# Kernel tuning notes

Measured on AMD Instinct MI355X. Metric: run time of the kernel, lower is better.

Reference implementation:

```python
import jax, jax.numpy as jnp
import numpy as np

N_NODES = 100000
N_EDGES = 1_600_000
F_IN, HID, N_CLS = 128, 64, 32
NEG_SLOPE = 0.2  # PyG GATv2Conv default


def _segment_softmax(scores, seg, num_segments):
    # numerically stable softmax over edges grouped by destination node
    m = jax.ops.segment_max(scores, seg, num_segments=num_segments)
    ex = jnp.exp(scores - m[seg])
    s = jax.ops.segment_sum(ex, seg, num_segments=num_segments)
    return ex / (s[seg] + 1e-16)


def _gatv2_layer(x, src, dst, Wl, bl, Wr, br, att, bias, num_nodes):
    xl = x @ Wl + bl              # source transform  [N, C]
    xr = x @ Wr + br              # target transform  [N, C]
    # per-edge GATv2 attention logit: a . leaky_relu(xl_j + xr_i)
    e = jax.nn.leaky_relu(xl[src] + xr[dst], NEG_SLOPE) @ att  # [E]
    alpha = _segment_softmax(e, dst, num_nodes)                 # [E]
    out = jax.ops.segment_sum(alpha[:, None] * xl[src], dst, num_segments=num_nodes)
    return out + bias


def _add_self_loops(edge_index, n):
    loops = jnp.arange(n, dtype=edge_index.dtype)
    return jnp.concatenate([edge_index, jnp.stack([loops, loops])], axis=1)


def setup_inputs() -> dict:
    key = jax.random.key(0)
    ks = jax.random.split(key, 8)
    s1 = 1.0 / np.sqrt(F_IN)
    s2 = 1.0 / np.sqrt(HID)
    return {
        "x": jax.random.normal(ks[0], (N_NODES, F_IN), jnp.float32),
        "edge_index": jax.random.randint(ks[1], (2, N_EDGES), 0, N_NODES, jnp.int64),
        "W1l": jax.random.normal(ks[2], (F_IN, HID), jnp.float32) * s1,
        "b1l": jnp.zeros((HID,), jnp.float32),
        "W1r": jax.random.normal(ks[3], (F_IN, HID), jnp.float32) * s1,
        "b1r": jnp.zeros((HID,), jnp.float32),
        "att1": jax.random.normal(ks[4], (HID,), jnp.float32) * s2,
        "bias1": jnp.zeros((HID,), jnp.float32),
        "W2l": jax.random.normal(ks[5], (HID, N_CLS), jnp.float32) * s2,
        "b2l": jnp.zeros((N_CLS,), jnp.float32),
        "W2r": jax.random.normal(ks[6], (HID, N_CLS), jnp.float32) * s2,
        "b2r": jnp.zeros((N_CLS,), jnp.float32),
        "att2": jax.random.normal(ks[7], (N_CLS,), jnp.float32) / np.sqrt(N_CLS),
        "bias2": jnp.zeros((N_CLS,), jnp.float32),
    }


def reference(x, edge_index, W1l, b1l, W1r, b1r, att1, bias1,
              W2l, b2l, W2r, b2r, att2, bias2):
    n = x.shape[0]
    ei = _add_self_loops(edge_index, n)
    src, dst = ei[0], ei[1]
    h = jax.nn.relu(_gatv2_layer(x, src, dst, W1l, b1l, W1r, b1r, att1, bias1, n))
    # F.dropout(training=False) is identity in eval mode
    out = _gatv2_layer(h, src, dst, W2l, b2l, W2r, b2r, att2, bias2, n)
    return out
```

## Files before the change

kernel.cpp:

```cpp
#include <hip/hip_runtime.h>
#include <math.h>

#define F_IN 128
#define HID 64
#define NCLS 32
#define NEG 0.2f
#define NBKT 256
#define CHUNK 8192

__device__ __forceinline__ void f4fma(float4& a, float s, const float4& w) {
    a.x = fmaf(s, w.x, a.x);
    a.y = fmaf(s, w.y, a.y);
    a.z = fmaf(s, w.z, a.z);
    a.w = fmaf(s, w.w, a.w);
}
__device__ __forceinline__ unsigned short f2bf(float f) {
    unsigned u = __float_as_uint(f);
    return (unsigned short)((u + 0x7FFFu + ((u >> 16) & 1u)) >> 16);
}
__device__ __forceinline__ float bf2f(unsigned short s) {
    return __uint_as_float(((unsigned)s) << 16);
}


__global__ __launch_bounds__(256) void zeroBuckets(int* __restrict__ bucketSize, int BK) {
    int i = blockIdx.x * 256 + threadIdx.x;
    if (i < BK) bucketSize[i] = 0;
}

__global__ __launch_bounds__(256) void bucketHist(const int* __restrict__ ei,
                                                  int Eorig, int Etot,
                                                  int* __restrict__ bucketSize, int BK) {
    __shared__ int h[512];
    int t = threadIdx.x;
    for (int j = t; j < BK; j += 256) h[j] = 0;
    __syncthreads();
    int base = blockIdx.x * CHUNK;
    int end = base + CHUNK < Etot ? base + CHUNK : Etot;
    for (int i = base + t; i < end; i += 256) {
        int dst = i < Eorig ? ei[Eorig + i] : i - Eorig;
        atomicAdd(&h[dst >> 8], 1);
    }
    __syncthreads();
    for (int j = t; j < BK; j += 256)
        if (h[j]) atomicAdd(&bucketSize[j], h[j]);
}

__global__ __launch_bounds__(256) void bucketScan(const int* __restrict__ bucketSize,
                                                  int* __restrict__ bucketStart,
                                                  int* __restrict__ bucketCursor,
                                                  int BK, int Etot) {
    __shared__ int sd[256];
    int t = threadIdx.x;
    int v0 = (2 * t     < BK) ? bucketSize[2 * t]     : 0;
    int v1 = (2 * t + 1 < BK) ? bucketSize[2 * t + 1] : 0;
    int ts = v0 + v1;
    sd[t] = ts;
    __syncthreads();
    for (int off = 1; off < 256; off <<= 1) {
        int x = (t >= off) ? sd[t - off] : 0;
        __syncthreads();
        sd[t] += x;
        __syncthreads();
    }
    int excl = sd[t] - ts;
    if (2 * t < BK)     { bucketStart[2 * t] = excl;          bucketCursor[2 * t] = excl; }
    if (2 * t + 1 < BK) { bucketStart[2 * t + 1] = excl + v0; bucketCursor[2 * t + 1] = excl + v0; }
    if (t == 255) bucketStart[BK] = Etot;
}

__global__ __launch_bounds__(256) void bucketScatter(const int* __restrict__ ei,
                                                     int Eorig, int Etot,
                                                     int* __restrict__ bucketCursor,
                                                     int2* __restrict__ pairs, int BK) {
    __shared__ int h[512], lbase[512], hcur[512];
    int t = threadIdx.x;
    for (int j = t; j < BK; j += 256) { h[j] = 0; hcur[j] = 0; }
    __syncthreads();
    int base = blockIdx.x * CHUNK;
    int end = base + CHUNK < Etot ? base + CHUNK : Etot;
    for (int i = base + t; i < end; i += 256) {
        int dst = i < Eorig ? ei[Eorig + i] : i - Eorig;
        atomicAdd(&h[dst >> 8], 1);
    }
    __syncthreads();
    for (int j = t; j < BK; j += 256)
        lbase[j] = h[j] ? atomicAdd(&bucketCursor[j], h[j]) : 0;
    __syncthreads();
    for (int i = base + t; i < end; i += 256) {
        int src, dst;
        if (i < Eorig) { src = ei[i]; dst = ei[Eorig + i]; }
        else           { src = dst = i - Eorig; }
        int b = dst >> 8;
        int off = atomicAdd(&hcur[b], 1);
        pairs[lbase[b] + off] = make_int2(src, dst);
    }
}

__global__ __launch_bounds__(256) void bucketCSR(const int2* __restrict__ pairs,
                                                 const int* __restrict__ bucketStart,
                                                 int* __restrict__ rowstart,
                                                 int* __restrict__ cnt,
                                                 int* __restrict__ srclist, int N) {
    __shared__ int c[256], cur[256];
    int t = threadIdx.x;
    int b = blockIdx.x;
    int lo = b * NBKT;
    int eb = bucketStart[b], ee = bucketStart[b + 1];
    c[t] = 0;
    __syncthreads();
    for (int i = eb + t; i < ee; i += 256)
        atomicAdd(&c[pairs[i].y - lo], 1);
    __syncthreads();
    cur[t] = c[t];
    __syncthreads();
    for (int off = 1; off < 256; off <<= 1) {
        int x = (t >= off) ? cur[t - off] : 0;
        __syncthreads();
        cur[t] += x;
        __syncthreads();
    }
    int excl = cur[t] - c[t];
    int node = lo + t;
    if (node < N) { rowstart[node] = eb + excl; cnt[node] = c[t]; }
    __syncthreads();
    cur[t] = excl;
    __syncthreads();
    for (int i = eb + t; i < ee; i += 256) {
        int2 pr = pairs[i];
        int pos = atomicAdd(&cur[pr.y - lo], 1);
        srclist[eb + pos] = pr.x;
    }
}

__global__ __launch_bounds__(256) void transform1(const float* __restrict__ x,
                                                  const float* __restrict__ Wl,
                                                  const float* __restrict__ bl,
                                                  const float* __restrict__ Wr,
                                                  const float* __restrict__ br,
                                                  unsigned short* __restrict__ xlb,
                                                  float* __restrict__ xr, int N) {
    __shared__ float sW[F_IN * HID];
    __shared__ float sx[64][132];
    const float* W = blockIdx.y ? Wr : Wl;
    const float* b = blockIdx.y ? br : bl;
    int t = threadIdx.x;
    int nb = blockIdx.x * 64;

#pragma unroll
    for (int j = 0; j < 8; j++) {
        int f = t + j * 256;
        ((float4*)sW)[f] = ((const float4*)W)[f];
    }
    int maxf = (N - nb) * 32;
#pragma unroll
    for (int j = 0; j < 8; j++) {
        int f = t + j * 256;
        int node = f >> 5, kc = f & 31;
        float4 v = {0.f, 0.f, 0.f, 0.f};
        if (f < maxf) v = ((const float4*)(x + (size_t)nb * F_IN))[f];
        *(float4*)&sx[node][kc * 4] = v;
    }
    __syncthreads();

    int c4 = (t & 15) * 4;
    int slot = t >> 4;
    float4 b4 = *(const float4*)(b + c4);
    float4 acc[4] = {b4, b4, b4, b4};

#pragma unroll 4
    for (int k4 = 0; k4 < F_IN / 4; k4++) {
        int k = k4 * 4;
        float4 w0 = *(const float4*)&sW[(k + 0) * HID + c4];
        float4 w1 = *(const float4*)&sW[(k + 1) * HID + c4];
        float4 w2 = *(const float4*)&sW[(k + 2) * HID + c4];
        float4 w3 = *(const float4*)&sW[(k + 3) * HID + c4];
#pragma unroll
        for (int j = 0; j < 4; j++) {
            float4 xv = *(const float4*)&sx[slot + j * 16][k];
            f4fma(acc[j], xv.x, w0);
            f4fma(acc[j], xv.y, w1);
            f4fma(acc[j], xv.z, w2);
            f4fma(acc[j], xv.w, w3);
        }
    }
    if (blockIdx.y) {
#pragma unroll
        for (int j = 0; j < 4; j++) {
            int g = nb + slot + j * 16;
            if (g < N) *(float4*)(xr + (size_t)g * HID + c4) = acc[j];
        }
    } else {
#pragma unroll
        for (int j = 0; j < 4; j++) {
            int g = nb + slot + j * 16;
            if (g < N) {
                ushort4 o;
                o.x = f2bf(acc[j].x); o.y = f2bf(acc[j].y);
                o.z = f2bf(acc[j].z); o.w = f2bf(acc[j].w);
                *(ushort4*)(xlb + (size_t)g * HID + c4) = o;
            }
        }
    }
}

__global__ __launch_bounds__(256) void transform2(const float* __restrict__ h,
                                                  const float* __restrict__ Wl,
                                                  const float* __restrict__ bl,
                                                  const float* __restrict__ Wr,
                                                  const float* __restrict__ br,
                                                  float* __restrict__ xl,
                                                  float* __restrict__ xr, int N) {
    __shared__ float sWl[HID * NCLS];
    __shared__ float sWr[HID * NCLS];
    __shared__ float sx[128][68];
    int t = threadIdx.x;
    int nb = blockIdx.x * 128;

#pragma unroll
    for (int j = 0; j < 2; j++) {
        int f = t + j * 256;
        ((float4*)sWl)[f] = ((const float4*)Wl)[f];
        ((float4*)sWr)[f] = ((const float4*)Wr)[f];
    }
    int maxf = (N - nb) * 16;
#pragma unroll
    for (int j = 0; j < 8; j++) {
        int f = t + j * 256;
        int node = f >> 4, kc = f & 15;
        float4 v = {0.f, 0.f, 0.f, 0.f};
        if (f < maxf) v = ((const float4*)(h + (size_t)nb * HID))[f];
        v.x = fmaxf(v.x, 0.f);
        v.y = fmaxf(v.y, 0.f);
        v.z = fmaxf(v.z, 0.f);
        v.w = fmaxf(v.w, 0.f);
        *(float4*)&sx[node][kc * 4] = v;
    }
    __syncthreads();

    int c4 = (t & 7) * 4;
    int slot = t >> 3;
    float4 bl4 = *(const float4*)(bl + c4);
    float4 br4 = *(const float4*)(br + c4);
    float4 accl[4] = {bl4, bl4, bl4, bl4};
    float4 accr[4] = {br4, br4, br4, br4};

#pragma unroll 4
    for (int k4 = 0; k4 < HID / 4; k4++) {
        int k = k4 * 4;
        float4 wl0 = *(const float4*)&sWl[(k + 0) * NCLS + c4];
        float4 wl1 = *(const float4*)&sWl[(k + 1) * NCLS + c4];
        float4 wl2 = *(const float4*)&sWl[(k + 2) * NCLS + c4];
        float4 wl3 = *(const float4*)&sWl[(k + 3) * NCLS + c4];
        float4 wr0 = *(const float4*)&sWr[(k + 0) * NCLS + c4];
        float4 wr1 = *(const float4*)&sWr[(k + 1) * NCLS + c4];
        float4 wr2 = *(const float4*)&sWr[(k + 2) * NCLS + c4];
        float4 wr3 = *(const float4*)&sWr[(k + 3) * NCLS + c4];
#pragma unroll
        for (int j = 0; j < 4; j++) {
            float4 xv = *(const float4*)&sx[slot + j * 32][k];
            f4fma(accl[j], xv.x, wl0); f4fma(accr[j], xv.x, wr0);
            f4fma(accl[j], xv.y, wl1); f4fma(accr[j], xv.y, wr1);
            f4fma(accl[j], xv.z, wl2); f4fma(accr[j], xv.z, wr2);
            f4fma(accl[j], xv.w, wl3); f4fma(accr[j], xv.w, wr3);
        }
    }
#pragma unroll
    for (int j = 0; j < 4; j++) {
        int g = nb + slot + j * 32;
        if (g < N) {
            *(float4*)(xl + (size_t)g * NCLS + c4) = accl[j];
            *(float4*)(xr + (size_t)g * NCLS + c4) = accr[j];
        }
    }
}

__global__ __launch_bounds__(256) void fusedAggB64(const unsigned short* __restrict__ xlb,
                                                   const float* __restrict__ xr,
                                                   const float* __restrict__ att,
                                                   const int* __restrict__ rowstart,
                                                   const int* __restrict__ cnt,
                                                   const int* __restrict__ srclist,
                                                   const float* __restrict__ bias,
                                                   float* __restrict__ out, int N) {
    const int C = HID, LPQ = 16, SLOTS = 4;
    int wid = threadIdx.x >> 6;
    int lane = threadIdx.x & 63;
    int n = blockIdx.x * 4 + wid;
    if (n >= N) return;

    int slot = lane / LPQ;
    int pos = lane % LPQ;
    int c4 = pos * 4;

    float4 xr4 = *(const float4*)(xr + (size_t)n * C + c4);
    float4 at4 = *(const float4*)(att + c4);
    float4 bi4 = *(const float4*)(bias + c4);

    int row = rowstart[n];
    int deg = cnt[n];

    float s = 0.f;
    float4 acc = {0.f, 0.f, 0.f, 0.f};

    for (int cb = 0; cb < deg; cb += 64) {
        int len = deg - cb; if (len > 64) len = 64;
        int li = lane < len ? lane : len - 1;
        int srcreg = srclist[row + cb + li];
        int nbatch = (len + SLOTS - 1) / SLOTS;
#pragma unroll 4
        for (int b = 0; b < nbatch; b++) {
            int eidx = b * SLOTS + slot;
            int src = __shfl(srcreg, eidx, 64);
            ushort4 q = *(const ushort4*)(xlb + (size_t)src * C + c4);
            float4 v;
            v.x = bf2f(q.x); v.y = bf2f(q.y); v.z = bf2f(q.z); v.w = bf2f(q.w);
            float4 u;
            u.x = v.x + xr4.x; u.y = v.y + xr4.y;
            u.z = v.z + xr4.z; u.w = v.w + xr4.w;
            u.x = fmaxf(u.x, NEG * u.x);
            u.y = fmaxf(u.y, NEG * u.y);
            u.z = fmaxf(u.z, NEG * u.z);
            u.w = fmaxf(u.w, NEG * u.w);
            float p = u.x * at4.x;
            p = fmaf(u.y, at4.y, p);
            p = fmaf(u.z, at4.z, p);
            p = fmaf(u.w, at4.w, p);
#pragma unroll
            for (int o = 1; o < LPQ; o <<= 1) p += __shfl_xor(p, o, 64);
            float w = (eidx < len) ? __expf(p) : 0.f;
            s += w;
            acc.x = fmaf(w, v.x, acc.x);
            acc.y = fmaf(w, v.y, acc.y);
            acc.z = fmaf(w, v.z, acc.z);
            acc.w = fmaf(w, v.w, acc.w);
        }
    }
#pragma unroll
    for (int o = LPQ; o < 64; o <<= 1) {
        acc.x += __shfl_xor(acc.x, o, 64);
        acc.y += __shfl_xor(acc.y, o, 64);
        acc.z += __shfl_xor(acc.z, o, 64);
        acc.w += __shfl_xor(acc.w, o, 64);
        s     += __shfl_xor(s,     o, 64);
    }
    if (lane < LPQ) {
        float inv = 1.f / (s + 1e-16f);
        float4 o4;
        o4.x = acc.x * inv + bi4.x;
        o4.y = acc.y * inv + bi4.y;
        o4.z = acc.z * inv + bi4.z;
        o4.w = acc.w * inv + bi4.w;
        *(float4*)(out + (size_t)n * C + c4) = o4;
    }
}

__global__ __launch_bounds__(256) void fusedAggF32(const float* __restrict__ xl,
                                                   const float* __restrict__ xr,
                                                   const float* __restrict__ att,
                                                   const int* __restrict__ rowstart,
                                                   const int* __restrict__ cnt,
                                                   const int* __restrict__ srclist,
                                                   const float* __restrict__ bias,
                                                   float* __restrict__ out, int N) {
    const int C = NCLS, LPQ = 8, SLOTS = 8;
    int wid = threadIdx.x >> 6;
    int lane = threadIdx.x & 63;
    int n = blockIdx.x * 4 + wid;
    if (n >= N) return;

    int slot = lane / LPQ;
    int pos = lane % LPQ;
    int c4 = pos * 4;

    float4 xr4 = *(const float4*)(xr + (size_t)n * C + c4);
    float4 at4 = *(const float4*)(att + c4);
    float4 bi4 = *(const float4*)(bias + c4);

    int row = rowstart[n];
    int deg = cnt[n];

    float s = 0.f;
    float4 acc = {0.f, 0.f, 0.f, 0.f};

    for (int cb = 0; cb < deg; cb += 64) {
        int len = deg - cb; if (len > 64) len = 64;
        int li = lane < len ? lane : len - 1;
        int srcreg = srclist[row + cb + li];
        int nbatch = (len + SLOTS - 1) / SLOTS;
#pragma unroll 4
        for (int b = 0; b < nbatch; b++) {
            int eidx = b * SLOTS + slot;
            int src = __shfl(srcreg, eidx, 64);
            float4 v = *(const float4*)(xl + (size_t)src * C + c4);
            float4 u;
            u.x = v.x + xr4.x; u.y = v.y + xr4.y;
            u.z = v.z + xr4.z; u.w = v.w + xr4.w;
            u.x = fmaxf(u.x, NEG * u.x);
            u.y = fmaxf(u.y, NEG * u.y);
            u.z = fmaxf(u.z, NEG * u.z);
            u.w = fmaxf(u.w, NEG * u.w);
            float p = u.x * at4.x;
            p = fmaf(u.y, at4.y, p);
            p = fmaf(u.z, at4.z, p);
            p = fmaf(u.w, at4.w, p);
#pragma unroll
            for (int o = 1; o < LPQ; o <<= 1) p += __shfl_xor(p, o, 64);
            float w = (eidx < len) ? __expf(p) : 0.f;
            s += w;
            acc.x = fmaf(w, v.x, acc.x);
            acc.y = fmaf(w, v.y, acc.y);
            acc.z = fmaf(w, v.z, acc.z);
            acc.w = fmaf(w, v.w, acc.w);
        }
    }
#pragma unroll
    for (int o = LPQ; o < 64; o <<= 1) {
        acc.x += __shfl_xor(acc.x, o, 64);
        acc.y += __shfl_xor(acc.y, o, 64);
        acc.z += __shfl_xor(acc.z, o, 64);
        acc.w += __shfl_xor(acc.w, o, 64);
        s     += __shfl_xor(s,     o, 64);
    }
    if (lane < LPQ) {
        float inv = 1.f / (s + 1e-16f);
        float4 o4;
        o4.x = acc.x * inv + bi4.x;
        o4.y = acc.y * inv + bi4.y;
        o4.z = acc.z * inv + bi4.z;
        o4.w = acc.w * inv + bi4.w;
        *(float4*)(out + (size_t)n * C + c4) = o4;
    }
}

extern "C" void kernel_launch(void* const* d_in, const int* in_sizes, int n_in,
                              void* d_out, int out_size, void* d_ws, size_t ws_size,
                              hipStream_t stream) {
    const float* x     = (const float*)d_in[0];
    const int*   ei    = (const int*)d_in[1];
    const float* W1l   = (const float*)d_in[2];
    const float* b1l   = (const float*)d_in[3];
    const float* W1r   = (const float*)d_in[4];
    const float* b1r   = (const float*)d_in[5];
    const float* att1  = (const float*)d_in[6];
    const float* bias1 = (const float*)d_in[7];
    const float* W2l   = (const float*)d_in[8];
    const float* b2l   = (const float*)d_in[9];
    const float* W2r   = (const float*)d_in[10];
    const float* b2r   = (const float*)d_in[11];
    const float* att2  = (const float*)d_in[12];
    const float* bias2 = (const float*)d_in[13];
    float* out = (float*)d_out;

    int N     = in_sizes[0] / F_IN;
    int Eorig = in_sizes[1] / 2;
    int Etot  = Eorig + N;
    int BK    = (N + NBKT - 1) / NBKT;

    char* p = (char*)d_ws;
    auto alloc = [&](size_t bytes) { void* r = (void*)p; p += (bytes + 255) & ~(size_t)255; return r; };
    unsigned short* xl1b = (unsigned short*)alloc((size_t)N * HID * 2);
    float* xr1     = (float*)alloc((size_t)N * HID * 4);
    float* h       = (float*)alloc((size_t)N * HID * 4);
    float* xl2     = (float*)alloc((size_t)N * NCLS * 4);
    float* xr2     = (float*)alloc((size_t)N * NCLS * 4);
    int*   cnt     = (int*)alloc((size_t)N * 4);
    int*   rowstart= (int*)alloc((size_t)N * 4);
    int*   srclist = (int*)alloc((size_t)Etot * 4);
    int*   bucketSize   = (int*)alloc(520 * 4);
    int*   bucketStart  = (int*)alloc(520 * 4);
    int*   bucketCursor = (int*)alloc(520 * 4);
    int2*  pairs   = (int2*)xl2;

    int nChunks = (Etot + CHUNK - 1) / CHUNK;

    zeroBuckets<<<2, 256, 0, stream>>>(bucketSize, BK);
    bucketHist<<<nChunks, 256, 0, stream>>>(ei, Eorig, Etot, bucketSize, BK);
    bucketScan<<<1, 256, 0, stream>>>(bucketSize, bucketStart, bucketCursor, BK, Etot);
    bucketScatter<<<nChunks, 256, 0, stream>>>(ei, Eorig, Etot, bucketCursor, pairs, BK);
    bucketCSR<<<BK, 256, 0, stream>>>(pairs, bucketStart, rowstart, cnt, srclist, N);

    transform1<<<dim3((N + 63) / 64, 2), 256, 0, stream>>>(x, W1l, b1l, W1r, b1r,
                                                           xl1b, xr1, N);
    fusedAggB64<<<(N + 3) / 4, 256, 0, stream>>>(xl1b, xr1, att1, rowstart, cnt,
                                                 srclist, bias1, h, N);

    transform2<<<(N + 127) / 128, 256, 0, stream>>>(h, W2l, b2l, W2r, b2r, xl2, xr2, N);
    fusedAggF32<<<(N + 3) / 4, 256, 0, stream>>>(xl2, xr2, att2, rowstart, cnt,
                                                 srclist, bias2, out, N);
}
```

Baseline: 346.6 us.

## Fuse left and right transforms in layer-1 GEMM with K-tiling

The layer-1 transform now computes both the source (Wl) and target (Wr) projections in a single block instead of launching a separate grid row for each. The goal is to read each x tile from global memory once rather than twice. The K dimension is split into two 64-wide tiles so shared memory stays about the same size, with both weight halves staged per tile. The cost is a second barrier, twice as many accumulator registers per thread, and half as many blocks launched.

```diff
diff --git a/kernel.cpp b/kernel.cpp
--- a/kernel.cpp
+++ b/kernel.cpp
@@ -140,66 +140,65 @@
                                                   const float* __restrict__ br,
                                                   unsigned short* __restrict__ xlb,
                                                   float* __restrict__ xr, int N) {
-    __shared__ float sW[F_IN * HID];
-    __shared__ float sx[64][132];
-    const float* W = blockIdx.y ? Wr : Wl;
-    const float* b = blockIdx.y ? br : bl;
+    __shared__ float sWl[64 * HID];
+    __shared__ float sWr[64 * HID];
+    __shared__ float sx[64][68];
     int t = threadIdx.x;
     int nb = blockIdx.x * 64;
-
-#pragma unroll
-    for (int j = 0; j < 8; j++) {
-        int f = t + j * 256;
-        ((float4*)sW)[f] = ((const float4*)W)[f];
-    }
-    int maxf = (N - nb) * 32;
-#pragma unroll
-    for (int j = 0; j < 8; j++) {
-        int f = t + j * 256;
-        int node = f >> 5, kc = f & 31;
-        float4 v = {0.f, 0.f, 0.f, 0.f};
-        if (f < maxf) v = ((const float4*)(x + (size_t)nb * F_IN))[f];
-        *(float4*)&sx[node][kc * 4] = v;
-    }
-    __syncthreads();
-
     int c4 = (t & 15) * 4;
     int slot = t >> 4;
-    float4 b4 = *(const float4*)(b + c4);
-    float4 acc[4] = {b4, b4, b4, b4};
+    int maxnode = N - nb;
+
+    float4 bl4 = *(const float4*)(bl + c4);
+    float4 br4 = *(const float4*)(br + c4);
+    float4 accl[4] = {bl4, bl4, bl4, bl4};
+    float4 accr[4] = {br4, br4, br4, br4};
+
+    for (int kt = 0; kt < 2; kt++) {
+        if (kt) __syncthreads();
+#pragma unroll
+        for (int j = 0; j < 4; j++) {
+            int f = t + j * 256;
+            ((float4*)sWl)[f] = ((const float4*)Wl)[kt * 1024 + f];
+            ((float4*)sWr)[f] = ((const float4*)Wr)[kt * 1024 + f];
+            int node = f >> 4, kc = f & 15;
+            float4 v = {0.f, 0.f, 0.f, 0.f};
+            if (node < maxnode)
+                v = ((const float4*)x)[(size_t)(nb + node) * 32 + kt * 16 + kc];
+            *(float4*)&sx[node][kc * 4] = v;
+        }
+        __syncthreads();
 
 #pragma unroll 4
-    for (int k4 = 0; k4 < F_IN / 4; k4++) {
-        int k = k4 * 4;
-        float4 w0 = *(const float4*)&sW[(k + 0) * HID + c4];
-        float4 w1 = *(const float4*)&sW[(k + 1) * HID + c4];
-        float4 w2 = *(const float4*)&sW[(k + 2) * HID + c4];
-        float4 w3 = *(const float4*)&sW[(k + 3) * HID + c4];
-#pragma unroll
-        for (int j = 0; j < 4; j++) {
-            float4 xv = *(const float4*)&sx[slot + j * 16][k];
-            f4fma(acc[j], xv.x, w0);
-            f4fma(acc[j], xv.y, w1);
-            f4fma(acc[j], xv.z, w2);
-            f4fma(acc[j], xv.w, w3);
-        }
-    }
-    if (blockIdx.y) {
-#pragma unroll
-        for (int j = 0; j < 4; j++) {
-            int g = nb + slot + j * 16;
-            if (g < N) *(float4*)(xr + (size_t)g * HID + c4) = acc[j];
-        }
-    } else {
-#pragma unroll
-        for (int j = 0; j < 4; j++) {
-            int g = nb + slot + j * 16;
-            if (g < N) {
-                ushort4 o;
-                o.x = f2bf(acc[j].x); o.y = f2bf(acc[j].y);
-                o.z = f2bf(acc[j].z); o.w = f2bf(acc[j].w);
-                *(ushort4*)(xlb + (size_t)g * HID + c4) = o;
+        for (int k4 = 0; k4 < 16; k4++) {
+            int k = k4 * 4;
+            float4 wl0 = *(const float4*)&sWl[(k + 0) * HID + c4];
+            float4 wl1 = *(const float4*)&sWl[(k + 1) * HID + c4];
+            float4 wl2 = *(const float4*)&sWl[(k + 2) * HID + c4];
+            float4 wl3 = *(const float4*)&sWl[(k + 3) * HID + c4];
+            float4 wr0 = *(const float4*)&sWr[(k + 0) * HID + c4];
+            float4 wr1 = *(const float4*)&sWr[(k + 1) * HID + c4];
+            float4 wr2 = *(const float4*)&sWr[(k + 2) * HID + c4];
+            float4 wr3 = *(const float4*)&sWr[(k + 3) * HID + c4];
+#pragma unroll
+            for (int j = 0; j < 4; j++) {
+                float4 xv = *(const float4*)&sx[slot + j * 16][k];
+                f4fma(accl[j], xv.x, wl0); f4fma(accr[j], xv.x, wr0);
+                f4fma(accl[j], xv.y, wl1); f4fma(accr[j], xv.y, wr1);
+                f4fma(accl[j], xv.z, wl2); f4fma(accr[j], xv.z, wr2);
+                f4fma(accl[j], xv.w, wl3); f4fma(accr[j], xv.w, wr3);
             }
+        }
+    }
+#pragma unroll
+    for (int j = 0; j < 4; j++) {
+        int g = nb + slot + j * 16;
+        if (g < N) {
+            ushort4 o;
+            o.x = f2bf(accl[j].x); o.y = f2bf(accl[j].y);
+            o.z = f2bf(accl[j].z); o.w = f2bf(accl[j].w);
+            *(ushort4*)(xlb + (size_t)g * HID + c4) = o;
+            *(float4*)(xr + (size_t)g * HID + c4) = accr[j];
         }
     }
 }
@@ -480,8 +479,7 @@
     bucketScatter<<<nChunks, 256, 0, stream>>>(ei, Eorig, Etot, bucketCursor, pairs, BK);
     bucketCSR<<<BK, 256, 0, stream>>>(pairs, bucketStart, rowstart, cnt, srclist, N);
 
-    transform1<<<dim3((N + 63) / 64, 2), 256, 0, stream>>>(x, W1l, b1l, W1r, b1r,
-                                                           xl1b, xr1, N);
+    transform1<<<(N + 63) / 64, 256, 0, stream>>>(x, W1l, b1l, W1r, b1r, xl1b, xr1, N);
     fusedAggB64<<<(N + 3) / 4, 256, 0, stream>>>(xl1b, xr1, att1, rowstart, cnt,
                                                  srclist, bias1, h, N);
 
```

Result: no change. 349.4 us (+0.8%).
